# Kernel tuning notes

Measured on AMD Instinct MI355X. Metric: run time of the kernel, lower is better.

Reference implementation:

```python
import jax, jax.numpy as jnp
import numpy as np

N, HID, MAXD, B, NCLS, GRUH = 50000, 128, 16, 50, 10, 32


def setup_inputs() -> dict:
    key = jax.random.key(0)
    ks = jax.random.split(key, 18)
    s = 0.05
    nrm = lambda k, shp: (jax.random.normal(k, shp, jnp.float32) * s)
    return {
        "feature": jax.random.normal(ks[0], (N, HID), jnp.float32),
        "nbr_idx": jax.random.randint(ks[1], (N, MAXD), 0, N, dtype=jnp.int32),
        "deg": jax.random.randint(ks[2], (N,), 1, MAXD + 1, dtype=jnp.int32),
        "graph_ids": (jnp.arange(N, dtype=jnp.int32) * B) // N,
        # SAGEConv(lstm) params: LSTM(in=HID, hidden=HID) + fc_self/fc_neigh
        "lstm_Wih": nrm(ks[3], (4 * HID, HID)),
        "lstm_Whh": nrm(ks[4], (4 * HID, HID)),
        "lstm_bih": nrm(ks[5], (4 * HID,)),
        "lstm_bhh": nrm(ks[6], (4 * HID,)),
        "W_self": nrm(ks[7], (HID, HID)),
        "W_neigh": nrm(ks[8], (HID, HID)),
        "b_sage": nrm(ks[9], (HID,)),
        # GraphConv params
        "W_gc": nrm(ks[10], (HID, HID)),
        "b_gc": nrm(ks[11], (HID,)),
        # GRU params (h0=0 so weight_hh contributes nothing; only its bias matters)
        "Wih_gru": nrm(ks[12], (3 * GRUH, HID)),
        "bih_gru": nrm(ks[13], (3 * GRUH,)),
        "bhh_gru": nrm(ks[14], (3 * GRUH,)),
        # classifier (dropout is identity at eval)
        "W_cls": nrm(ks[15], (GRUH, NCLS)),
        "b_cls": nrm(ks[16], (NCLS,)),
    }


def _lstm_aggregate(feats, nbr_idx, deg, Wih, Whh, bih, bhh):
    # DGL SAGEConv 'lstm' reducer: run LSTM over each node's neighbor features,
    # take final hidden state. Implemented as a masked scan over padded lists.
    n, hdim = feats.shape
    h0 = jnp.zeros((n, hdim), feats.dtype)

    def step(carry, t):
        h, c = carry
        x = feats[jnp.take(nbr_idx, t, axis=1)]  # [N, HID] gather of t-th neighbor
        gates = x @ Wih.T + bih + h @ Whh.T + bhh
        i, f, g, o = jnp.split(gates, 4, axis=-1)  # torch gate order i,f,g,o
        c_new = jax.nn.sigmoid(f) * c + jax.nn.sigmoid(i) * jnp.tanh(g)
        h_new = jax.nn.sigmoid(o) * jnp.tanh(c_new)
        valid = (t < deg)[:, None]
        return (jnp.where(valid, h_new, h), jnp.where(valid, c_new, c)), None

    (hT, _), _ = jax.lax.scan(step, (h0, h0), jnp.arange(nbr_idx.shape[1]))
    return hT  # hidden at each node's last valid neighbor


def _graph_conv(h, nbr_idx, deg, W, b):
    # DGL GraphConv norm='both': D^-1/2 A D^-1/2 h W + b
    n, maxd = nbr_idx.shape
    norm = jax.lax.rsqrt(jnp.maximum(deg.astype(h.dtype), 1.0))
    hn = h * norm[:, None]
    mask = (jnp.arange(maxd, dtype=jnp.int32)[None, :] < deg[:, None]).astype(h.dtype)
    contrib = hn[nbr_idx.reshape(-1)] * mask.reshape(-1)[:, None]  # [N*MAXD, HID]
    dst = jnp.repeat(jnp.arange(n, dtype=jnp.int32), maxd)
    agg = jax.ops.segment_sum(contrib, dst, num_segments=n)
    return (agg * norm[:, None]) @ W + b


def _gru_step(x, Wih, bih, bhh):
    # single GRU step with h0 = 0 (seq_len == 1 in the original view(1, N, H))
    gh = x @ Wih.T + bih  # [N, 3*GRUH]
    xr, xz, xn = jnp.split(gh, 3, axis=-1)  # torch gate order r,z,n
    br, bz, bn = jnp.split(bhh, 3)
    r = jax.nn.sigmoid(xr + br)
    z = jax.nn.sigmoid(xz + bz)
    nst = jnp.tanh(xn + r * bn)
    return (1.0 - z) * nst  # h' = (1-z)*n + z*h0, h0 = 0


def reference(feature, nbr_idx, deg, graph_ids, lstm_Wih, lstm_Whh, lstm_bih,
              lstm_bhh, W_self, W_neigh, b_sage, W_gc, b_gc, Wih_gru, bih_gru,
              bhh_gru, W_cls, b_cls):
    # conv4: SAGEConv lstm -> relu
    h_nei = _lstm_aggregate(feature, nbr_idx, deg, lstm_Wih, lstm_Whh, lstm_bih, lstm_bhh)
    h = jax.nn.relu(feature @ W_self + h_nei @ W_neigh + b_sage)
    # conv2: GraphConv -> relu
    h = jax.nn.relu(_graph_conv(h, nbr_idx, deg, W_gc, b_gc))
    # GRU over seq_len=1, batch=N
    out = _gru_step(h, Wih_gru, bih_gru, bhh_gru)  # [N, 32]
    # dgl.mean_nodes: per-graph mean pool
    sums = jax.ops.segment_sum(out, graph_ids, num_segments=B)
    cnts = jax.ops.segment_sum(jnp.ones((out.shape[0],), out.dtype), graph_ids, num_segments=B)
    hg = sums / cnts[:, None]
    # classify (Dropout is identity in eval)
    return hg @ W_cls + b_cls  # [B, NCLS]
```

## Files before the change

### kernel.cpp

```cpp
#include <hip/hip_runtime.h>
#include <hip/hip_bf16.h>


#define NN     50000
#define HIDD   128
#define MAXD   16
#define NGRAPH 50
#define NCLSS  10
#define GRUH   32

typedef __attribute__((ext_vector_type(8))) short s16x8;
typedef __attribute__((ext_vector_type(4))) float f32x4;
typedef __hip_bfloat16 bf16;

#define MFMA16(a,b,c)  __builtin_amdgcn_mfma_f32_16x16x32_bf16((a),(b),(c),0,0,0)

__device__ __forceinline__ float bf2f(bf16 x) { return __bfloat162float(x); }
__device__ __forceinline__ bf16  f2bf(float x) { return __float2bfloat16(x); }
__device__ __forceinline__ s16x8 ldfrag(const bf16* p) { return *(const s16x8*)p; }

__device__ __forceinline__ float sigf(float x) {
  return __builtin_amdgcn_rcpf(1.0f + __expf(-x));
}
__device__ __forceinline__ float tanhf_(float x) {
  return 1.0f - 2.0f * __builtin_amdgcn_rcpf(1.0f + __expf(2.0f * x));
}

__device__ __forceinline__ void lgkm_barrier() {
  asm volatile("s_waitcnt lgkmcnt(0)\n\ts_barrier" ::: "memory");
}

__global__ void prep_kernel(const float* __restrict__ feat, const float* __restrict__ Wih,
                            const float* __restrict__ Whh, const float* __restrict__ bih,
                            const float* __restrict__ bhh, const float* __restrict__ Wself,
                            const float* __restrict__ Wneigh, const float* __restrict__ Wgc,
                            const float* __restrict__ Wgru,
                            bf16* featB, bf16* WihB, bf16* WhhB, bf16* WsT, bf16* WnT,
                            bf16* WgT, bf16* WgruB, float* biasS) {
  const int nf = NN * HIDD;
  const int total = nf + 2 * 65536 + 3 * 16384 + 12288 + 512;
  int stride = gridDim.x * blockDim.x;
  for (int idx = blockIdx.x * blockDim.x + threadIdx.x; idx < total; idx += stride) {
    if (idx < nf) { featB[idx] = f2bf(feat[idx]); continue; }
    int j = idx - nf;
    if (j < 65536) { WihB[j] = f2bf(Wih[j]); continue; }
    j -= 65536;
    if (j < 65536) { WhhB[j] = f2bf(Whh[j]); continue; }
    j -= 65536;
    if (j < 16384) { int c = j >> 7, k = j & 127; WsT[j] = f2bf(Wself[k * HIDD + c]); continue; }
    j -= 16384;
    if (j < 16384) { int c = j >> 7, k = j & 127; WnT[j] = f2bf(Wneigh[k * HIDD + c]); continue; }
    j -= 16384;
    if (j < 16384) { int c = j >> 7, k = j & 127; WgT[j] = f2bf(Wgc[k * HIDD + c]); continue; }
    j -= 16384;
    if (j < 12288) { WgruB[j] = f2bf(Wgru[j]); continue; }
    j -= 12288;
    biasS[j] = bih[j] + bhh[j];
  }
}

__global__ __launch_bounds__(256) void hist_kernel(const int* __restrict__ deg, int* hist) {
  __shared__ int lh[17];
  const int tid = threadIdx.x;
  if (tid < 17) lh[tid] = 0;
  __syncthreads();
  const int i = blockIdx.x * 256 + tid;
  if (i < NN) atomicAdd(&lh[deg[i]], 1);
  __syncthreads();
  if (tid < 17 && lh[tid]) atomicAdd(&hist[tid], lh[tid]);
}

__global__ __launch_bounds__(256) void scatter_kernel(const int* __restrict__ deg,
                                                      const int* __restrict__ hist,
                                                      int* __restrict__ resv,
                                                      int* __restrict__ perm) {
  __shared__ int lh[17], lbase[17], lpos[17];
  const int tid = threadIdx.x;
  if (tid < 17) { lh[tid] = 0; lpos[tid] = 0; }
  __syncthreads();
  const int i = blockIdx.x * 256 + tid;
  const int d = (i < NN) ? deg[i] : -1;
  if (d >= 0) atomicAdd(&lh[d], 1);
  __syncthreads();
  if (tid < 17) {
    int pre = 0;
    for (int k = tid + 1; k < 17; ++k) pre += hist[k];
    lbase[tid] = pre + (lh[tid] ? atomicAdd(&resv[tid], lh[tid]) : 0);
  }
  __syncthreads();
  if (d >= 0) {
    const int p = lbase[d] + atomicAdd(&lpos[d], 1);
    perm[p] = i;
  }
}

__global__ __launch_bounds__(512, 2) void lstm_kernel(const bf16* __restrict__ featB,
                                                      const bf16* __restrict__ WihB,
                                                      const bf16* __restrict__ WhhB,
                                                      const float* __restrict__ biasS,
                                                      const int* __restrict__ nbr_idx,
                                                      const int* __restrict__ deg,
                                                      const int* __restrict__ perm,
                                                      bf16* __restrict__ hTB) {
  __shared__ __align__(16) bf16 Xs[2][32 * 128];
  __shared__ __align__(16) bf16 Hs[2][32 * 128];
  __shared__ int nbr_s[16 * 32];
  __shared__ int nodes_s[32];
  __shared__ int degs_s[32];

  const int tid = threadIdx.x;
  const int lane = tid & 63, w = tid >> 6;
  const int l15 = lane & 15, quad = lane >> 4;
  const int base = blockIdx.x * 32;
  const int colw = w * 16 + l15;
  const int srow = tid >> 4, schk = tid & 15;

  if (tid < 32) {
    const int gi = base + tid;
    const int nd = (gi < NN) ? perm[gi] : -1;
    nodes_s[tid] = nd;
    degs_s[tid] = (nd >= 0) ? deg[nd] : 0;
  }
  __syncthreads();
  for (int e = tid; e < 16 * 32; e += 512) {
    const int row = e & 31, t = e >> 5;
    const int nd = nodes_s[row];
    nbr_s[t * 32 + row] = (nd >= 0) ? nbr_idx[nd * MAXD + t] : 0;
  }

  s16x8 Bh[4][4], Bi[4][4];
#pragma unroll
  for (int q = 0; q < 4; ++q)
#pragma unroll
    for (int kt = 0; kt < 4; ++kt) {
      Bh[q][kt] = ldfrag(WhhB + (q * 128 + colw) * HIDD + kt * 32 + quad * 8);
      asm volatile("" : "+v"(Bh[q][kt]));
      Bi[q][kt] = ldfrag(WihB + (q * 128 + colw) * HIDD + kt * 32 + quad * 8);
      asm volatile("" : "+v"(Bi[q][kt]));
    }
  float biasv[4];
#pragma unroll
  for (int q = 0; q < 4; ++q) biasv[q] = biasS[q * 128 + colw];

  __syncthreads();
  const int maxdeg = degs_s[0];

  int mydeg[2][4];
#pragma unroll
  for (int rt = 0; rt < 2; ++rt)
#pragma unroll
    for (int rr = 0; rr < 4; ++rr) mydeg[rt][rr] = degs_s[rt * 16 + quad * 4 + rr];

  {
    const int nb0 = nbr_s[0 * 32 + srow];
    *(s16x8*)(Xs[0] + srow * 128 + ((schk ^ (srow & 15)) * 8)) =
        ldfrag(featB + (size_t)nb0 * HIDD + schk * 8);
  }
  float cst[2][4] = {{0.f, 0.f, 0.f, 0.f}, {0.f, 0.f, 0.f, 0.f}};
  float hprev[2][4] = {{0.f, 0.f, 0.f, 0.f}, {0.f, 0.f, 0.f, 0.f}};
  lgkm_barrier();

  for (int t = 0; t < maxdeg; ++t) {
    const int cur = t & 1, nxt = cur ^ 1;
    s16x8 xstage;
    const bool do_stage = (t + 1 < maxdeg);
    if (do_stage) {
      const int nb1 = nbr_s[(t + 1) * 32 + srow];
      xstage = ldfrag(featB + (size_t)nb1 * HIDD + schk * 8);
    }

    f32x4 acc[2][4];
#pragma unroll
    for (int rt = 0; rt < 2; ++rt)
#pragma unroll
      for (int q = 0; q < 4; ++q) acc[rt][q] = (f32x4){0.f, 0.f, 0.f, 0.f};

#pragma unroll
    for (int kt = 0; kt < 4; ++kt) {
      const int oct = kt * 4 + quad;
      const s16x8 ax0 = ldfrag(Xs[cur] + (0 * 16 + l15) * 128 + ((oct ^ l15) * 8));
      const s16x8 ax1 = ldfrag(Xs[cur] + (1 * 16 + l15) * 128 + ((oct ^ l15) * 8));
#pragma unroll
      for (int q = 0; q < 4; ++q) {
        acc[0][q] = MFMA16(ax0, Bi[q][kt], acc[0][q]);
        acc[1][q] = MFMA16(ax1, Bi[q][kt], acc[1][q]);
      }
    }

    if (t > 0) {
#pragma unroll
      for (int rt = 0; rt < 2; ++rt)
#pragma unroll
        for (int kt = 0; kt < 4; ++kt) {
          const int m = rt * 16 + l15;
          const int oct = kt * 4 + quad;
          const s16x8 ah = ldfrag(Hs[cur] + m * 128 + ((oct ^ l15) * 8));
#pragma unroll
          for (int q = 0; q < 4; ++q)
            acc[rt][q] = MFMA16(ah, Bh[q][kt], acc[rt][q]);
        }
    }

#pragma unroll
    for (int rt = 0; rt < 2; ++rt)
#pragma unroll
      for (int rr = 0; rr < 4; ++rr) {
        const int row = rt * 16 + quad * 4 + rr;
        const float g_i = acc[rt][0][rr] + biasv[0];
        const float g_f = acc[rt][1][rr] + biasv[1];
        const float g_g = acc[rt][2][rr] + biasv[2];
        const float g_o = acc[rt][3][rr] + biasv[3];
        const float iv = sigf(g_i), fv = sigf(g_f);
        const float gv = tanhf_(g_g), ov = sigf(g_o);
        const float cn = fv * cst[rt][rr] + iv * gv;
        const float hn_new = ov * tanhf_(cn);
        const bool act = (t < mydeg[rt][rr]);
        if (act) cst[rt][rr] = cn;
        const float hn = act ? hn_new : hprev[rt][rr];
        hprev[rt][rr] = hn;
        Hs[nxt][row * 128 + (((colw >> 3) ^ (row & 15)) * 8) + (colw & 7)] = f2bf(hn);
      }
    if (do_stage)
      *(s16x8*)(Xs[nxt] + srow * 128 + ((schk ^ (srow & 15)) * 8)) = xstage;

    lgkm_barrier();
  }

  const bf16* Hf = Hs[maxdeg & 1];
  for (int e = tid; e < 32 * 16; e += 512) {
    const int row = e >> 4, j = e & 15;
    const int nd = nodes_s[row];
    if (nd >= 0) {
      const s16x8 v = ldfrag(Hf + row * 128 + ((j ^ (row & 15)) * 8));
      *(s16x8*)(hTB + (size_t)nd * HIDD + j * 8) = v;
    }
  }
}

__global__ __launch_bounds__(256) void sage_kernel(const bf16* __restrict__ featB,
                                                   const bf16* __restrict__ hTB,
                                                   const bf16* __restrict__ WsT,
                                                   const bf16* __restrict__ WnT,
                                                   const float* __restrict__ b_sage,
                                                   const int* __restrict__ deg,
                                                   bf16* __restrict__ h1n) {
  const int lane = threadIdx.x & 63, wave = threadIdx.x >> 6;
  const int l15 = lane & 15, quad = lane >> 4;
  const int nb = blockIdx.x * 64 + wave * 16;
  int arow = nb + l15; if (arow >= NN) arow = NN - 1;
  s16x8 Fa[4], Ha[4];
#pragma unroll
  for (int kt = 0; kt < 4; ++kt) {
    Fa[kt] = ldfrag(featB + (size_t)arow * HIDD + kt * 32 + quad * 8);
    Ha[kt] = ldfrag(hTB + (size_t)arow * HIDD + kt * 32 + quad * 8);
  }
  int nodes[4]; float nrm[4];
#pragma unroll
  for (int r = 0; r < 4; ++r) {
    const int nd = nb + quad * 4 + r;
    nodes[r] = nd;
    nrm[r] = rsqrtf((float)deg[(nd < NN) ? nd : (NN - 1)]);
  }
  for (int ct = 0; ct < 8; ++ct) {
    const int col = ct * 16 + l15;
    f32x4 acc = {0.f, 0.f, 0.f, 0.f};
#pragma unroll
    for (int kt = 0; kt < 4; ++kt) {
      acc = MFMA16(Fa[kt], ldfrag(WsT + col * HIDD + kt * 32 + quad * 8), acc);
      acc = MFMA16(Ha[kt], ldfrag(WnT + col * HIDD + kt * 32 + quad * 8), acc);
    }
    const float bb = b_sage[col];
#pragma unroll
    for (int r = 0; r < 4; ++r)
      if (nodes[r] < NN) {
        const float v = fmaxf(acc[r] + bb, 0.f) * nrm[r];
        h1n[(size_t)nodes[r] * HIDD + col] = f2bf(v);
      }
  }
}

__global__ __launch_bounds__(256) void agg_kernel(const bf16* __restrict__ h1n,
                                                  const int* __restrict__ nbr_idx,
                                                  const int* __restrict__ deg,
                                                  bf16* __restrict__ aggB) {
  const int wave = threadIdx.x >> 6, lane = threadIdx.x & 63;
  const int node = blockIdx.x * 4 + wave;
  if (node >= NN) return;
  const int d = deg[node];
  const int idx_l = nbr_idx[node * MAXD + (lane & 15)];
  const int c = lane * 2;
  float a0 = 0.f, a1 = 0.f;
  for (int t = 0; t < d; ++t) {
    const int nbr = __shfl(idx_l, t, 64);
    const __hip_bfloat162 v = *(const __hip_bfloat162*)(h1n + (size_t)nbr * HIDD + c);
    a0 += __bfloat162float(v.x);
    a1 += __bfloat162float(v.y);
  }
  const float nm = rsqrtf((float)d);
  aggB[(size_t)node * HIDD + c]     = f2bf(a0 * nm);
  aggB[(size_t)node * HIDD + c + 1] = f2bf(a1 * nm);
}

__global__ __launch_bounds__(256) void gcgru_kernel(const bf16* __restrict__ aggB,
                                                    const bf16* __restrict__ WgT,
                                                    const float* __restrict__ b_gc,
                                                    const bf16* __restrict__ WgruB,
                                                    const float* __restrict__ bih,
                                                    const float* __restrict__ bhh,
                                                    float* __restrict__ gout) {
  __shared__ __align__(16) bf16 H2[64 * 136];
  const int lane = threadIdx.x & 63, wave = threadIdx.x >> 6;
  const int l15 = lane & 15, quad = lane >> 4;
  const int nb = blockIdx.x * 64 + wave * 16;
  int arow = nb + l15; if (arow >= NN) arow = NN - 1;
  s16x8 A[4];
#pragma unroll
  for (int kt = 0; kt < 4; ++kt) A[kt] = ldfrag(aggB + (size_t)arow * HIDD + kt * 32 + quad * 8);
  for (int ct = 0; ct < 8; ++ct) {
    const int col = ct * 16 + l15;
    f32x4 acc = {0.f, 0.f, 0.f, 0.f};
#pragma unroll
    for (int kt = 0; kt < 4; ++kt)
      acc = MFMA16(A[kt], ldfrag(WgT + col * HIDD + kt * 32 + quad * 8), acc);
    const float bb = b_gc[col];
#pragma unroll
    for (int r = 0; r < 4; ++r)
      H2[(wave * 16 + quad * 4 + r) * 136 + col] = f2bf(fmaxf(acc[r] + bb, 0.f));
  }
  __syncthreads();
  s16x8 A2[4];
#pragma unroll
  for (int kt = 0; kt < 4; ++kt)
    A2[kt] = ldfrag(H2 + (wave * 16 + l15) * 136 + kt * 32 + quad * 8);
  f32x4 acc[6];
#pragma unroll
  for (int ct = 0; ct < 6; ++ct) {
    f32x4 a = {0.f, 0.f, 0.f, 0.f};
#pragma unroll
    for (int kt = 0; kt < 4; ++kt)
      a = MFMA16(A2[kt], ldfrag(WgruB + (ct * 16 + l15) * HIDD + kt * 32 + quad * 8), a);
    acc[ct] = a;
  }
#pragma unroll
  for (int u = 0; u < 2; ++u) {
    const int cu = 16 * u + l15;
    const float br = bih[cu] + bhh[cu];
    const float bz = bih[32 + cu] + bhh[32 + cu];
    const float bni = bih[64 + cu];
    const float bnh = bhh[64 + cu];
#pragma unroll
    for (int r = 0; r < 4; ++r) {
      const int node = nb + quad * 4 + r;
      if (node < NN) {
        const float rv = sigf(acc[u][r] + br);
        const float zv = sigf(acc[2 + u][r] + bz);
        const float nv = tanhf_(acc[4 + u][r] + bni + rv * bnh);
        gout[(size_t)node * GRUH + cu] = (1.f - zv) * nv;
      }
    }
  }
}

#define POOL_CHUNK 512
__global__ __launch_bounds__(256) void pool_partial_kernel(const float* __restrict__ gout,
                                                           const int* __restrict__ gids,
                                                           float* __restrict__ sums,
                                                           float* __restrict__ cnts) {
  __shared__ float ls[NGRAPH * GRUH];
  __shared__ float lc[NGRAPH];
  const int tid = threadIdx.x;
  for (int i = tid; i < NGRAPH * GRUH; i += 256) ls[i] = 0.f;
  if (tid < NGRAPH) lc[tid] = 0.f;
  __syncthreads();

  const int wave = tid >> 6, lane = tid & 63;
  const int c = lane & 31, half = lane >> 5;
  const int base = blockIdx.x * POOL_CHUNK + wave * (POOL_CHUNK / 8);

  float accv = 0.f, ccnt = 0.f;
  int curg = -1;
  for (int it = 0; it < POOL_CHUNK / 16; ++it) {
    const int n = base + it * 2 + half;
    if (n < NN) {
      const int g = gids[n];
      const float v = gout[(size_t)n * GRUH + c];
      if (g != curg) {
        if (curg >= 0) {
          atomicAdd(&ls[curg * GRUH + c], accv);
          if (c == 0) atomicAdd(&lc[curg], ccnt);
        }
        curg = g; accv = 0.f; ccnt = 0.f;
      }
      accv += v; ccnt += 1.f;
    }
  }
  if (curg >= 0) {
    atomicAdd(&ls[curg * GRUH + c], accv);
    if (c == 0) atomicAdd(&lc[curg], ccnt);
  }
  __syncthreads();
  for (int i = tid; i < NGRAPH * GRUH; i += 256)
    if (ls[i] != 0.f) atomicAdd(&sums[i], ls[i]);
  if (tid < NGRAPH && lc[tid] != 0.f) atomicAdd(&cnts[tid], lc[tid]);
}

__global__ __launch_bounds__(256) void pool_final_kernel(const float* __restrict__ sums,
                                                         const float* __restrict__ cnts,
                                                         const float* __restrict__ Wcls,
                                                         const float* __restrict__ bcls,
                                                         float* __restrict__ out) {
  const int idx = blockIdx.x * blockDim.x + threadIdx.x;
  if (idx >= NGRAPH * NCLSS) return;
  const int g = idx / NCLSS, k = idx % NCLSS;
  const float inv = 1.0f / cnts[g];
  float acc = bcls[k];
#pragma unroll
  for (int cc = 0; cc < GRUH; ++cc)
    acc += sums[g * GRUH + cc] * inv * Wcls[cc * NCLSS + k];
  out[idx] = acc;
}

extern "C" void kernel_launch(void* const* d_in, const int* in_sizes, int n_in,
                              void* d_out, int out_size, void* d_ws, size_t ws_size,
                              hipStream_t stream) {
  const float* feature  = (const float*)d_in[0];
  const int*   nbr_idx  = (const int*)d_in[1];
  const int*   deg      = (const int*)d_in[2];
  const int*   gids     = (const int*)d_in[3];
  const float* lstm_Wih = (const float*)d_in[4];
  const float* lstm_Whh = (const float*)d_in[5];
  const float* lstm_bih = (const float*)d_in[6];
  const float* lstm_bhh = (const float*)d_in[7];
  const float* W_self   = (const float*)d_in[8];
  const float* W_neigh  = (const float*)d_in[9];
  const float* b_sage   = (const float*)d_in[10];
  const float* W_gc     = (const float*)d_in[11];
  const float* b_gc     = (const float*)d_in[12];
  const float* Wih_gru  = (const float*)d_in[13];
  const float* bih_gru  = (const float*)d_in[14];
  const float* bhh_gru  = (const float*)d_in[15];
  const float* W_cls    = (const float*)d_in[16];
  const float* b_cls    = (const float*)d_in[17];

  char* ws = (char*)d_ws;
  bf16*  featB = (bf16*)(ws + 0);
  bf16*  hTB   = (bf16*)(ws + 12800000);
  bf16*  h1nB  = (bf16*)(ws + 25600000);
  bf16*  aggB  = (bf16*)(ws + 38400000);
  float* gout  = (float*)(ws + 12800000);
  const size_t wo = 64000000;
  bf16*  WihB  = (bf16*)(ws + wo);
  bf16*  WhhB  = (bf16*)(ws + wo + 131072);
  bf16*  WsT   = (bf16*)(ws + wo + 262144);
  bf16*  WnT   = (bf16*)(ws + wo + 294912);
  bf16*  WgT   = (bf16*)(ws + wo + 327680);
  bf16*  WgruB = (bf16*)(ws + wo + 360448);
  float* biasS = (float*)(ws + wo + 385024);
  int*   perm  = (int*)(ws + 65000000);
  int*   hist  = (int*)(ws + 65400000);
  int*   resv  = hist + 17;
  float* psums = (float*)(ws + 65401216);
  float* pcnts = psums + NGRAPH * GRUH;

  prep_kernel<<<3072, 256, 0, stream>>>(feature, lstm_Wih, lstm_Whh, lstm_bih, lstm_bhh,
                                        W_self, W_neigh, W_gc, Wih_gru,
                                        featB, WihB, WhhB, WsT, WnT, WgT, WgruB, biasS);
  hipMemsetAsync(hist, 0, 34 * sizeof(int), stream);
  hipMemsetAsync(psums, 0, (NGRAPH * GRUH + NGRAPH) * sizeof(float), stream);
  hist_kernel<<<196, 256, 0, stream>>>(deg, hist);
  scatter_kernel<<<196, 256, 0, stream>>>(deg, hist, resv, perm);
  lstm_kernel<<<1563, 512, 0, stream>>>(featB, WihB, WhhB, biasS, nbr_idx, deg, perm, hTB);
  sage_kernel<<<782, 256, 0, stream>>>(featB, hTB, WsT, WnT, b_sage, deg, h1nB);
  agg_kernel<<<12500, 256, 0, stream>>>(h1nB, nbr_idx, deg, aggB);
  gcgru_kernel<<<782, 256, 0, stream>>>(aggB, WgT, b_gc, WgruB, bih_gru, bhh_gru, gout);
  pool_partial_kernel<<<(NN + POOL_CHUNK - 1) / POOL_CHUNK, 256, 0, stream>>>(gout, gids, psums, pcnts);
  pool_final_kernel<<<2, 256, 0, stream>>>(psums, pcnts, W_cls, b_cls, (float*)d_out);
}
```

Before: 422.8 us.

## Precompute LSTM input projection per node once, gather gate preactivations in recurrence

The input-to-hidden LSTM projection is hoisted out of the recurrence. A new GEMM kernel computes x@Wih^T+bias once per node (50k rows) into a bf16 gate buffer, and the LSTM loop gathers each neighbor's precomputed 512-wide gate row instead of recomputing it for every (node, step). This removes about half of the MFMA work in the serial loop and the per-step feature staging through LDS. In exchange it adds a 51 MB bf16 intermediate write and heavier random gathers per step (1 KB per neighbor instead of 256 B). The LSTM block also grows to 64 rows with 1024 threads, and sage now reads fp32 features directly so the workspace can be reused.

```diff
diff --git a/kernel.cpp b/kernel.cpp
--- a/kernel.cpp
+++ b/kernel.cpp
@@ -19,12 +19,29 @@
 __device__ __forceinline__ bf16  f2bf(float x) { return __float2bfloat16(x); }
 __device__ __forceinline__ s16x8 ldfrag(const bf16* p) { return *(const s16x8*)p; }
 
+__device__ __forceinline__ s16x8 ldfrag_f32(const float* p) {
+  const float4 a = *(const float4*)p;
+  const float4 b = *(const float4*)(p + 4);
+  union { s16x8 v; bf16 h[8]; } r;
+  r.h[0] = f2bf(a.x); r.h[1] = f2bf(a.y); r.h[2] = f2bf(a.z); r.h[3] = f2bf(a.w);
+  r.h[4] = f2bf(b.x); r.h[5] = f2bf(b.y); r.h[6] = f2bf(b.z); r.h[7] = f2bf(b.w);
+  return r.v;
+}
+
 __device__ __forceinline__ float sigf(float x) {
   return __builtin_amdgcn_rcpf(1.0f + __expf(-x));
 }
 __device__ __forceinline__ float tanhf_(float x) {
   return 1.0f - 2.0f * __builtin_amdgcn_rcpf(1.0f + __expf(2.0f * x));
 }
+
+__device__ __forceinline__ unsigned packbf2(float a, float b) {
+  union { bf16 h; unsigned short u; } x, y;
+  x.h = f2bf(a); y.h = f2bf(b);
+  return (unsigned)x.u | ((unsigned)y.u << 16);
+}
+__device__ __forceinline__ float lo2f(unsigned u) { return __uint_as_float(u << 16); }
+__device__ __forceinline__ float hi2f(unsigned u) { return __uint_as_float(u & 0xffff0000u); }
 
 __device__ __forceinline__ void lgkm_barrier() {
   asm volatile("s_waitcnt lgkmcnt(0)\n\ts_barrier" ::: "memory");
@@ -94,141 +111,161 @@
   }
 }
 
-__global__ __launch_bounds__(512, 2) void lstm_kernel(const bf16* __restrict__ featB,
-                                                      const bf16* __restrict__ WihB,
-                                                      const bf16* __restrict__ WhhB,
-                                                      const float* __restrict__ biasS,
-                                                      const int* __restrict__ nbr_idx,
-                                                      const int* __restrict__ deg,
-                                                      const int* __restrict__ perm,
-                                                      bf16* __restrict__ hTB) {
-  __shared__ __align__(16) bf16 Xs[2][32 * 128];
-  __shared__ __align__(16) bf16 Hs[2][32 * 128];
-  __shared__ int nbr_s[16 * 32];
-  __shared__ int nodes_s[32];
-  __shared__ int degs_s[32];
+__global__ __launch_bounds__(256) void ggemm_kernel(const bf16* __restrict__ featB,
+                                                    const bf16* __restrict__ WihB,
+                                                    const float* __restrict__ biasS,
+                                                    bf16* __restrict__ Gp) {
+  const int lane = threadIdx.x & 63, wave = threadIdx.x >> 6;
+  const int l15 = lane & 15, quad = lane >> 4;
+  const int nb = blockIdx.x * 64;
+
+  s16x8 Bx[4][4];
+#pragma unroll
+  for (int nt = 0; nt < 4; ++nt) {
+    int arow = nb + nt * 16 + l15; if (arow >= NN) arow = NN - 1;
+#pragma unroll
+    for (int kt = 0; kt < 4; ++kt)
+      Bx[nt][kt] = ldfrag(featB + (size_t)arow * HIDD + kt * 32 + quad * 8);
+  }
+
+  for (int hg = wave * 8; hg < wave * 8 + 8; ++hg) {
+    const int wr = (l15 & 3) * HIDD + hg * 4 + (l15 >> 2);
+    s16x8 Aw[4];
+#pragma unroll
+    for (int kt = 0; kt < 4; ++kt)
+      Aw[kt] = ldfrag(WihB + (size_t)wr * HIDD + kt * 32 + quad * 8);
+    const int hcol = hg * 4 + quad;
+    float b0 = biasS[0 * HIDD + hcol], b1 = biasS[1 * HIDD + hcol];
+    float b2 = biasS[2 * HIDD + hcol], b3 = biasS[3 * HIDD + hcol];
+#pragma unroll
+    for (int nt = 0; nt < 4; ++nt) {
+      f32x4 acc = {0.f, 0.f, 0.f, 0.f};
+#pragma unroll
+      for (int kt = 0; kt < 4; ++kt)
+        acc = MFMA16(Aw[kt], Bx[nt][kt], acc);
+      const int node = nb + nt * 16 + l15;
+      if (node < NN) {
+        unsigned u0 = packbf2(acc[0] + b0, acc[1] + b1);
+        unsigned u1 = packbf2(acc[2] + b2, acc[3] + b3);
+        *(uint2*)(Gp + (size_t)node * 512 + hcol * 4) = make_uint2(u0, u1);
+      }
+    }
+  }
+}
+
+__global__ __launch_bounds__(1024, 4) void lstm_kernel(const bf16* __restrict__ Gp,
+                                                       const bf16* __restrict__ WhhB,
+                                                       const int* __restrict__ nbr_idx,
+                                                       const int* __restrict__ deg,
+                                                       const int* __restrict__ perm,
+                                                       bf16* __restrict__ hTB) {
+  __shared__ __align__(16) bf16 Hs[2][64 * 128];
+  __shared__ int nbr_s[16 * 64];
+  __shared__ int nodes_s[64];
+  __shared__ int degs_s[64];
 
   const int tid = threadIdx.x;
   const int lane = tid & 63, w = tid >> 6;
   const int l15 = lane & 15, quad = lane >> 4;
-  const int base = blockIdx.x * 32;
-  const int colw = w * 16 + l15;
-  const int srow = tid >> 4, schk = tid & 15;
-
-  if (tid < 32) {
+  const int base = blockIdx.x * 64;
+
+  if (tid < 64) {
     const int gi = base + tid;
     const int nd = (gi < NN) ? perm[gi] : -1;
     nodes_s[tid] = nd;
     degs_s[tid] = (nd >= 0) ? deg[nd] : 0;
   }
   __syncthreads();
-  for (int e = tid; e < 16 * 32; e += 512) {
-    const int row = e & 31, t = e >> 5;
+  {
+    const int row = tid & 63, t = tid >> 6;
     const int nd = nodes_s[row];
-    nbr_s[t * 32 + row] = (nd >= 0) ? nbr_idx[nd * MAXD + t] : 0;
-  }
-
-  s16x8 Bh[4][4], Bi[4][4];
-#pragma unroll
-  for (int q = 0; q < 4; ++q)
+    nbr_s[t * 64 + row] = (nd >= 0) ? nbr_idx[nd * MAXD + t] : 0;
+  }
+
+  s16x8 Bh[2][4];
+#pragma unroll
+  for (int gt = 0; gt < 2; ++gt) {
+    const int wr = (l15 & 3) * HIDD + w * 8 + gt * 4 + (l15 >> 2);
 #pragma unroll
     for (int kt = 0; kt < 4; ++kt) {
-      Bh[q][kt] = ldfrag(WhhB + (q * 128 + colw) * HIDD + kt * 32 + quad * 8);
-      asm volatile("" : "+v"(Bh[q][kt]));
-      Bi[q][kt] = ldfrag(WihB + (q * 128 + colw) * HIDD + kt * 32 + quad * 8);
-      asm volatile("" : "+v"(Bi[q][kt]));
-    }
-  float biasv[4];
-#pragma unroll
-  for (int q = 0; q < 4; ++q) biasv[q] = biasS[q * 128 + colw];
+      Bh[gt][kt] = ldfrag(WhhB + (size_t)wr * HIDD + kt * 32 + quad * 8);
+      asm volatile("" : "+v"(Bh[gt][kt]));
+    }
+  }
 
   __syncthreads();
   const int maxdeg = degs_s[0];
 
-  int mydeg[2][4];
-#pragma unroll
-  for (int rt = 0; rt < 2; ++rt)
-#pragma unroll
-    for (int rr = 0; rr < 4; ++rr) mydeg[rt][rr] = degs_s[rt * 16 + quad * 4 + rr];
-
-  {
-    const int nb0 = nbr_s[0 * 32 + srow];
-    *(s16x8*)(Xs[0] + srow * 128 + ((schk ^ (srow & 15)) * 8)) =
-        ldfrag(featB + (size_t)nb0 * HIDD + schk * 8);
-  }
+  int mydeg[4];
+#pragma unroll
+  for (int nt = 0; nt < 4; ++nt) mydeg[nt] = degs_s[nt * 16 + l15];
+
+  const int gofs0 = (w * 8 + 0 * 4 + quad) * 4;
+  const int gofs1 = (w * 8 + 1 * 4 + quad) * 4;
+
   float cst[2][4] = {{0.f, 0.f, 0.f, 0.f}, {0.f, 0.f, 0.f, 0.f}};
   float hprev[2][4] = {{0.f, 0.f, 0.f, 0.f}, {0.f, 0.f, 0.f, 0.f}};
-  lgkm_barrier();
 
   for (int t = 0; t < maxdeg; ++t) {
     const int cur = t & 1, nxt = cur ^ 1;
-    s16x8 xstage;
-    const bool do_stage = (t + 1 < maxdeg);
-    if (do_stage) {
-      const int nb1 = nbr_s[(t + 1) * 32 + srow];
-      xstage = ldfrag(featB + (size_t)nb1 * HIDD + schk * 8);
+
+    uint2 gx[2][4];
+#pragma unroll
+    for (int nt = 0; nt < 4; ++nt) {
+      const int nb1 = nbr_s[t * 64 + nt * 16 + l15];
+      const bf16* gr = Gp + (size_t)nb1 * 512;
+      gx[0][nt] = *(const uint2*)(gr + gofs0);
+      gx[1][nt] = *(const uint2*)(gr + gofs1);
     }
 
     f32x4 acc[2][4];
 #pragma unroll
-    for (int rt = 0; rt < 2; ++rt)
-#pragma unroll
-      for (int q = 0; q < 4; ++q) acc[rt][q] = (f32x4){0.f, 0.f, 0.f, 0.f};
-
-#pragma unroll
-    for (int kt = 0; kt < 4; ++kt) {
-      const int oct = kt * 4 + quad;
-      const s16x8 ax0 = ldfrag(Xs[cur] + (0 * 16 + l15) * 128 + ((oct ^ l15) * 8));
-      const s16x8 ax1 = ldfrag(Xs[cur] + (1 * 16 + l15) * 128 + ((oct ^ l15) * 8));
-#pragma unroll
-      for (int q = 0; q < 4; ++q) {
-        acc[0][q] = MFMA16(ax0, Bi[q][kt], acc[0][q]);
-        acc[1][q] = MFMA16(ax1, Bi[q][kt], acc[1][q]);
+    for (int gt = 0; gt < 2; ++gt)
+#pragma unroll
+      for (int nt = 0; nt < 4; ++nt) acc[gt][nt] = (f32x4){0.f, 0.f, 0.f, 0.f};
+
+    if (t > 0) {
+#pragma unroll
+      for (int kt = 0; kt < 4; ++kt) {
+#pragma unroll
+        for (int nt = 0; nt < 4; ++nt) {
+          const int row = nt * 16 + l15;
+          const s16x8 ah = ldfrag(Hs[cur] + row * 128 + (((kt * 4 + quad) ^ l15) * 8));
+#pragma unroll
+          for (int gt = 0; gt < 2; ++gt)
+            acc[gt][nt] = MFMA16(Bh[gt][kt], ah, acc[gt][nt]);
+        }
       }
     }
 
-    if (t > 0) {
-#pragma unroll
-      for (int rt = 0; rt < 2; ++rt)
-#pragma unroll
-        for (int kt = 0; kt < 4; ++kt) {
-          const int m = rt * 16 + l15;
-          const int oct = kt * 4 + quad;
-          const s16x8 ah = ldfrag(Hs[cur] + m * 128 + ((oct ^ l15) * 8));
-#pragma unroll
-          for (int q = 0; q < 4; ++q)
-            acc[rt][q] = MFMA16(ah, Bh[q][kt], acc[rt][q]);
-        }
-    }
-
-#pragma unroll
-    for (int rt = 0; rt < 2; ++rt)
-#pragma unroll
-      for (int rr = 0; rr < 4; ++rr) {
-        const int row = rt * 16 + quad * 4 + rr;
-        const float g_i = acc[rt][0][rr] + biasv[0];
-        const float g_f = acc[rt][1][rr] + biasv[1];
-        const float g_g = acc[rt][2][rr] + biasv[2];
-        const float g_o = acc[rt][3][rr] + biasv[3];
+#pragma unroll
+    for (int gt = 0; gt < 2; ++gt) {
+      const int col = w * 8 + gt * 4 + quad;
+#pragma unroll
+      for (int nt = 0; nt < 4; ++nt) {
+        const int row = nt * 16 + l15;
+        const uint2 g = gx[gt][nt];
+        const float g_i = acc[gt][nt][0] + lo2f(g.x);
+        const float g_f = acc[gt][nt][1] + hi2f(g.x);
+        const float g_g = acc[gt][nt][2] + lo2f(g.y);
+        const float g_o = acc[gt][nt][3] + hi2f(g.y);
         const float iv = sigf(g_i), fv = sigf(g_f);
         const float gv = tanhf_(g_g), ov = sigf(g_o);
-        const float cn = fv * cst[rt][rr] + iv * gv;
+        const float cn = fv * cst[gt][nt] + iv * gv;
         const float hn_new = ov * tanhf_(cn);
-        const bool act = (t < mydeg[rt][rr]);
-        if (act) cst[rt][rr] = cn;
-        const float hn = act ? hn_new : hprev[rt][rr];
-        hprev[rt][rr] = hn;
-        Hs[nxt][row * 128 + (((colw >> 3) ^ (row & 15)) * 8) + (colw & 7)] = f2bf(hn);
+        const bool act = (t < mydeg[nt]);
+        if (act) cst[gt][nt] = cn;
+        const float hn = act ? hn_new : hprev[gt][nt];
+        hprev[gt][nt] = hn;
+        Hs[nxt][row * 128 + ((w ^ (row & 15)) * 8) + (col & 7)] = f2bf(hn);
       }
-    if (do_stage)
-      *(s16x8*)(Xs[nxt] + srow * 128 + ((schk ^ (srow & 15)) * 8)) = xstage;
-
+    }
     lgkm_barrier();
   }
 
   const bf16* Hf = Hs[maxdeg & 1];
-  for (int e = tid; e < 32 * 16; e += 512) {
-    const int row = e >> 4, j = e & 15;
+  {
+    const int row = tid >> 4, j = tid & 15;
     const int nd = nodes_s[row];
     if (nd >= 0) {
       const s16x8 v = ldfrag(Hf + row * 128 + ((j ^ (row & 15)) * 8));
@@ -237,7 +274,7 @@
   }
 }
 
-__global__ __launch_bounds__(256) void sage_kernel(const bf16* __restrict__ featB,
+__global__ __launch_bounds__(256) void sage_kernel(const float* __restrict__ featF,
                                                    const bf16* __restrict__ hTB,
                                                    const bf16* __restrict__ WsT,
                                                    const bf16* __restrict__ WnT,
@@ -251,7 +288,7 @@
   s16x8 Fa[4], Ha[4];
 #pragma unroll
   for (int kt = 0; kt < 4; ++kt) {
-    Fa[kt] = ldfrag(featB + (size_t)arow * HIDD + kt * 32 + quad * 8);
+    Fa[kt] = ldfrag_f32(featF + (size_t)arow * HIDD + kt * 32 + quad * 8);
     Ha[kt] = ldfrag(hTB + (size_t)arow * HIDD + kt * 32 + quad * 8);
   }
   int nodes[4]; float nrm[4];
@@ -444,10 +481,11 @@
 
   char* ws = (char*)d_ws;
   bf16*  featB = (bf16*)(ws + 0);
-  bf16*  hTB   = (bf16*)(ws + 12800000);
-  bf16*  h1nB  = (bf16*)(ws + 25600000);
-  bf16*  aggB  = (bf16*)(ws + 38400000);
-  float* gout  = (float*)(ws + 12800000);
+  bf16*  hTB   = (bf16*)(ws + 0);
+  float* gout  = (float*)(ws + 0);
+  bf16*  Gp    = (bf16*)(ws + 12800000);
+  bf16*  h1nB  = (bf16*)(ws + 12800000);
+  bf16*  aggB  = (bf16*)(ws + 25600000);
   const size_t wo = 64000000;
   bf16*  WihB  = (bf16*)(ws + wo);
   bf16*  WhhB  = (bf16*)(ws + wo + 131072);
@@ -456,10 +494,10 @@
   bf16*  WgT   = (bf16*)(ws + wo + 327680);
   bf16*  WgruB = (bf16*)(ws + wo + 360448);
   float* biasS = (float*)(ws + wo + 385024);
-  int*   perm  = (int*)(ws + 65000000);
-  int*   hist  = (int*)(ws + 65400000);
+  int*   perm  = (int*)(ws + 64500000);
+  int*   hist  = (int*)(ws + 64800000);
   int*   resv  = hist + 17;
-  float* psums = (float*)(ws + 65401216);
+  float* psums = (float*)(ws + 64801216);
   float* pcnts = psums + NGRAPH * GRUH;
 
   prep_kernel<<<3072, 256, 0, stream>>>(feature, lstm_Wih, lstm_Whh, lstm_bih, lstm_bhh,
@@ -469,8 +507,9 @@
   hipMemsetAsync(psums, 0, (NGRAPH * GRUH + NGRAPH) * sizeof(float), stream);
   hist_kernel<<<196, 256, 0, stream>>>(deg, hist);
   scatter_kernel<<<196, 256, 0, stream>>>(deg, hist, resv, perm);
-  lstm_kernel<<<1563, 512, 0, stream>>>(featB, WihB, WhhB, biasS, nbr_idx, deg, perm, hTB);
-  sage_kernel<<<782, 256, 0, stream>>>(featB, hTB, WsT, WnT, b_sage, deg, h1nB);
+  ggemm_kernel<<<782, 256, 0, stream>>>(featB, WihB, biasS, Gp);
+  lstm_kernel<<<782, 1024, 0, stream>>>(Gp, WhhB, nbr_idx, deg, perm, hTB);
+  sage_kernel<<<782, 256, 0, stream>>>(feature, hTB, WsT, WnT, b_sage, deg, h1nB);
   agg_kernel<<<12500, 256, 0, stream>>>(h1nB, nbr_idx, deg, aggB);
   gcgru_kernel<<<782, 256, 0, stream>>>(aggB, WgT, b_gc, WgruB, bih_gru, bhh_gru, gout);
   pool_partial_kernel<<<(NN + POOL_CHUNK - 1) / POOL_CHUNK, 256, 0, stream>>>(gout, gids, psums, pcnts);
```

Measured after the change: 441.8 us. 1.04x slower.
